# Optimization experiments

Hardware: AMD Instinct MI355X
Metric: run time of the kernel (lower is better)

## Reference

```python
import jax, jax.numpy as jnp
import numpy as np
from jax.ops import segment_sum

N_NODES = 100000


def gcn_conv(x, W, b, src, dst, num_nodes):
    # PyG GCNConv: h = x @ W; add self-loops; symmetric normalization; aggregate; + bias
    h = x @ W  # [N, out]
    # add self-loops
    loops = jnp.arange(num_nodes, dtype=src.dtype)
    src_sl = jnp.concatenate([src, loops])
    dst_sl = jnp.concatenate([dst, loops])
    # degree over destination (incl. self-loops), edge weight = 1
    deg = segment_sum(jnp.ones_like(src_sl, dtype=h.dtype), dst_sl, num_segments=num_nodes)
    dinv = jnp.where(deg > 0, jax.lax.rsqrt(deg), 0.0)
    norm = dinv[src_sl] * dinv[dst_sl]  # [E+N]
    msg = h[src_sl] * norm[:, None]      # gather + scale, [E+N, out]
    out = segment_sum(msg, dst_sl, num_segments=num_nodes)  # scatter-add
    return out + b


def setup_inputs() -> dict:
    key = jax.random.key(0)
    ks = jax.random.split(key, 5)
    N, F, C = N_NODES, 64, 10
    E = 1600000
    x = jax.random.normal(ks[0], (N, F), dtype=jnp.float32)
    edge_index = jax.random.randint(ks[1], (2, E), 0, N, dtype=jnp.int64)
    W1 = jax.random.normal(ks[2], (F, 128), dtype=jnp.float32) * (1.0 / np.sqrt(F))
    b1 = jnp.zeros((128,), dtype=jnp.float32)
    W2 = jax.random.normal(ks[3], (128, 16), dtype=jnp.float32) * (1.0 / np.sqrt(128))
    b2 = jnp.zeros((16,), dtype=jnp.float32)
    Wl = jax.random.normal(ks[4], (16, C), dtype=jnp.float32) * (1.0 / np.sqrt(16))
    bl = jnp.zeros((C,), dtype=jnp.float32)
    return {"x": x, "edge_index": edge_index, "W1": W1, "b1": b1,
            "W2": W2, "b2": b2, "Wl": Wl, "bl": bl}


def reference(x, edge_index, W1, b1, W2, b2, Wl, bl):
    src, dst = edge_index[0], edge_index[1]
    h = gcn_conv(x, W1, b1, src, dst, N_NODES)
    h = jax.nn.relu(h)
    h = gcn_conv(h, W2, b2, src, dst, N_NODES)
    h = jax.nn.relu(h)
    return h @ Wl + bl
```

## Files before the change

kernel.cpp:

```cpp
#include <hip/hip_runtime.h>
#include <hip/hip_fp16.h>


#define F_IN 64
#define H1DIM 128
#define H2DIM 16
#define C_OUT 10

#define NB 1024
#define BSZ_LOG 7
#define SC_PER_TH 16

typedef _Float16 f16x8 __attribute__((ext_vector_type(8)));
typedef _Float16 f16x4 __attribute__((ext_vector_type(4)));
typedef float f32x4 __attribute__((ext_vector_type(4)));

__global__ void bucket_count(const int* __restrict__ ei, int E,
                             int* __restrict__ bucket_cnt) {
    __shared__ int h[NB];
    for (int t = threadIdx.x; t < NB; t += blockDim.x) h[t] = 0;
    __syncthreads();
    int stride = gridDim.x * blockDim.x;
    for (int e = blockIdx.x * blockDim.x + threadIdx.x; e < E; e += stride) {
        int d = ei[E + e];
        atomicAdd(&h[d >> BSZ_LOG], 1);
    }
    __syncthreads();
    for (int t = threadIdx.x; t < NB; t += blockDim.x)
        if (h[t]) atomicAdd(&bucket_cnt[t], h[t]);
}

__global__ void bucket_scan(const int* __restrict__ bucket_cnt,
                            int* __restrict__ bucket_off,
                            int* __restrict__ bucket_cursor) {
    __shared__ int sh[NB];
    int tid = threadIdx.x;
    int v = bucket_cnt[tid];
    sh[tid] = v;
    __syncthreads();
#pragma unroll
    for (int off = 1; off < NB; off <<= 1) {
        int t = (tid >= off) ? sh[tid - off] : 0;
        __syncthreads();
        sh[tid] += t;
        __syncthreads();
    }
    int ex = sh[tid] - v;
    bucket_off[tid] = ex;
    bucket_cursor[tid] = ex;
    if (tid == NB - 1) bucket_off[NB] = sh[tid];
}

__global__ __launch_bounds__(256) void bucket_scatter(
        const int* __restrict__ ei, int E,
        int* __restrict__ bucket_cursor, unsigned long long* __restrict__ pairs) {
    __shared__ int cnt[NB];
    __shared__ int base[NB];
    for (int t = threadIdx.x; t < NB; t += 256) cnt[t] = 0;
    __syncthreads();

    long long chunk = (long long)blockIdx.x * (256 * SC_PER_TH);
    int s_[SC_PER_TH], d_[SC_PER_TH];
    int m = 0;
#pragma unroll
    for (int k = 0; k < SC_PER_TH; k++) {
        long long e = chunk + k * 256 + threadIdx.x;
        if (e < E) { s_[m] = ei[e]; d_[m] = ei[E + e]; m++; }
    }
    for (int k = 0; k < m; k++) atomicAdd(&cnt[d_[k] >> BSZ_LOG], 1);
    __syncthreads();
    for (int t = threadIdx.x; t < NB; t += 256) {
        int c = cnt[t];
        base[t] = c ? atomicAdd(&bucket_cursor[t], c) : 0;
        cnt[t] = 0;
    }
    __syncthreads();
    for (int k = 0; k < m; k++) {
        int b = d_[k] >> BSZ_LOG;
        int pos = base[b] + atomicAdd(&cnt[b], 1);
        pairs[pos] = ((unsigned long long)(unsigned)d_[k] << 32) | (unsigned)s_[k];
    }
}

__global__ __launch_bounds__(256) void build_csr_convert(
        const unsigned long long* __restrict__ pairs,
        const int* __restrict__ bucket_off,
        const float* __restrict__ x, int N,
        float* __restrict__ dinv, int* __restrict__ row_off,
        int* __restrict__ csr_src, __half2* __restrict__ xh2) {
    int b = blockIdx.x;
    int base_node = b << BSZ_LOG;
    int nn = min(128, N - base_node);
    __shared__ int cnt[128];
    __shared__ int sc[128];
    __shared__ int cur[128];
    __shared__ float sdi[128];
    int tid = threadIdx.x;
    if (tid < 128) cnt[tid] = 0;
    __syncthreads();

    int pbeg = bucket_off[b], pend = bucket_off[b + 1];
    for (int j = pbeg + tid; j < pend; j += 256)
        atomicAdd(&cnt[(int)(pairs[j] >> 32) - base_node], 1);
    __syncthreads();

    int v = (tid < 128) ? cnt[tid] : 0;
    if (tid < 128) sc[tid] = v;
    __syncthreads();
#pragma unroll
    for (int off = 1; off < 128; off <<= 1) {
        int t = (tid < 128 && tid >= off) ? sc[tid - off] : 0;
        __syncthreads();
        if (tid < 128) sc[tid] += t;
        __syncthreads();
    }
    if (tid < nn) {
        int ro = pbeg + sc[tid] - v;
        row_off[base_node + tid] = ro;
        cur[tid] = ro;
        float di = rsqrtf((float)(v + 1));
        dinv[base_node + tid] = di;
        sdi[tid] = di;
    }
    if (b == 0 && tid == 0) row_off[N] = bucket_off[NB];
    __syncthreads();

    for (int j = pbeg + tid; j < pend; j += 256) {
        unsigned long long p = pairs[j];
        int d = (int)(p >> 32), s = (int)(p & 0xffffffffu);
        int pos = atomicAdd(&cur[d - base_node], 1);
        csr_src[pos] = s;
    }

    const float2* x2 = (const float2*)x;
    int total = nn * 32;
    for (int t = tid; t < total; t += 256) {
        int nl = t >> 5, l = t & 31;
        float di = sdi[nl];
        long long idx = (long long)(base_node + nl) * 32 + l;
        float2 xv = x2[idx];
        xh2[idx] = __floats2half2_rn(xv.x * di, xv.y * di);
    }
}

__global__ __launch_bounds__(256) void gather1_h2(
        const f16x8* __restrict__ xh8, const float* __restrict__ dinv,
        const int* __restrict__ row_off, const int* __restrict__ csr_src,
        int N, f16x8* __restrict__ agg1h8) {
    int node = (blockIdx.x * 256 + threadIdx.x) >> 3;
    if (node >= N) return;
    int p = threadIdx.x & 7;
    int beg = row_off[node], end = row_off[node + 1];
    f16x8 self = xh8[(size_t)node * 8 + p];
    float acc[8];
#pragma unroll
    for (int q = 0; q < 8; q++) acc[q] = (float)self[q];
    int j = beg;
    for (; j + 4 <= end; j += 4) {
        int s0 = csr_src[j], s1 = csr_src[j + 1];
        int s2 = csr_src[j + 2], s3 = csr_src[j + 3];
        f16x8 v0 = xh8[(size_t)s0 * 8 + p];
        f16x8 v1 = xh8[(size_t)s1 * 8 + p];
        f16x8 v2 = xh8[(size_t)s2 * 8 + p];
        f16x8 v3 = xh8[(size_t)s3 * 8 + p];
#pragma unroll
        for (int q = 0; q < 8; q++)
            acc[q] += ((float)v0[q] + (float)v1[q]) + ((float)v2[q] + (float)v3[q]);
    }
    for (; j < end; ++j) {
        f16x8 v = xh8[(size_t)csr_src[j] * 8 + p];
#pragma unroll
        for (int q = 0; q < 8; q++) acc[q] += (float)v[q];
    }
    float di = dinv[node];
    f16x8 o;
#pragma unroll
    for (int q = 0; q < 8; q++) o[q] = (_Float16)(acc[q] * di);
    agg1h8[(size_t)node * 8 + p] = o;
}

__global__ __launch_bounds__(256) void pack_weights(
        const float* __restrict__ W1, const float* __restrict__ W2,
        f16x8* __restrict__ W1p, f16x8* __restrict__ W2p) {
    int s = blockIdx.x * 256 + threadIdx.x;
    if (s < 1024) {
        int frag = s >> 6, lane = s & 63;
        int tile = frag >> 1, kf = frag & 1;
        int c = lane & 15, g = lane >> 4;
        f16x8 v;
#pragma unroll
        for (int j = 0; j < 8; ++j)
            v[j] = (_Float16)W1[(kf * 32 + g * 8 + j) * H1DIM + tile * 16 + c];
        W1p[s] = v;
    } else if (s < 1024 + 256) {
        int s2 = s - 1024;
        int f = s2 >> 6, lane = s2 & 63;
        int c = lane & 15, g = lane >> 4;
        f16x8 v;
#pragma unroll
        for (int j = 0; j < 8; ++j)
            v[j] = (_Float16)W2[(f * 32 + g * 8 + j) * H2DIM + c];
        W2p[s2] = v;
    }
}

__global__ __launch_bounds__(256) void dense1_mfma(
        const _Float16* __restrict__ agg, const f16x8* __restrict__ W1p,
        const f16x8* __restrict__ W2p, const float* __restrict__ b1,
        const float* __restrict__ dinv, int N, _Float16* __restrict__ z2h) {
    __shared__ float sb1[H1DIM];
    __shared__ _Float16 Hl[4][16 * H1DIM];
    if (threadIdx.x < H1DIM) sb1[threadIdx.x] = b1[threadIdx.x];
    __syncthreads();
    const int wave = threadIdx.x >> 6, lane = threadIdx.x & 63;
    const int c = lane & 15, g = lane >> 4;
    const int nodeBase = blockIdx.x * 64 + wave * 16;

    int nld = nodeBase + c; if (nld > N - 1) nld = N - 1;
    const f16x8 a0 = *(const f16x8*)(agg + (size_t)nld * 64 + g * 8);
    const f16x8 a1 = *(const f16x8*)(agg + (size_t)nld * 64 + 32 + g * 8);

    _Float16* hl = Hl[wave];
    const f32x4 zero = {0.f, 0.f, 0.f, 0.f};
#pragma unroll
    for (int t = 0; t < 8; ++t) {
        f32x4 d = __builtin_amdgcn_mfma_f32_16x16x32_f16(W1p[(t * 2 + 1) * 64 + lane], a1, zero, 0, 0, 0);
        d = __builtin_amdgcn_mfma_f32_16x16x32_f16(W1p[(t * 2 + 0) * 64 + lane], a0, d, 0, 0, 0);
        f16x4 hv;
#pragma unroll
        for (int r = 0; r < 4; ++r)
            hv[r] = (_Float16)fmaxf(d[r] + sb1[t * 16 + g * 4 + r], 0.f);
        unsigned byte = ((unsigned)c * 256 + (unsigned)t * 32 + (unsigned)g * 8) ^ ((unsigned)(c & 7) << 4);
        *(f16x4*)((char*)hl + byte) = hv;
    }

    f32x4 acc = zero;
#pragma unroll
    for (int f = 0; f < 4; ++f) {
        unsigned byte = ((unsigned)c * 256 + (unsigned)f * 64 + (unsigned)g * 16) ^ ((unsigned)(c & 7) << 4);
        f16x8 a2 = *(const f16x8*)((char*)hl + byte);
        acc = __builtin_amdgcn_mfma_f32_16x16x32_f16(a2, W2p[f * 64 + lane], acc, 0, 0, 0);
    }
#pragma unroll
    for (int r = 0; r < 4; ++r) {
        int node = nodeBase + g * 4 + r;
        if (node < N) z2h[(size_t)node * 16 + c] = (_Float16)(acc[r] * dinv[node]);
    }
}

__global__ __launch_bounds__(256) void gather2_final_v2(
        const __half2* __restrict__ z2h, const float* __restrict__ dinv,
        const int* __restrict__ row_off, const int* __restrict__ csr_src,
        const float* __restrict__ b2, const float* __restrict__ Wl,
        const float* __restrict__ bl, int N, float* __restrict__ out) {
    __shared__ float sWl[H2DIM * C_OUT];
    __shared__ float sb2[H2DIM];
    __shared__ float sbl[C_OUT];
    __shared__ float hbuf[32][17];
    int tid = threadIdx.x;
    if (tid < H2DIM * C_OUT) sWl[tid] = Wl[tid];
    if (tid < H2DIM) sb2[tid] = b2[tid];
    if (tid < C_OUT) sbl[tid] = bl[tid];
    __syncthreads();

    int node = blockIdx.x * 32 + (tid >> 3);
    int p = tid & 7;
    int ln = tid >> 3;
    if (node < N) {
        int beg = row_off[node], end = row_off[node + 1];
        float2 sv = __half22float2(z2h[(size_t)node * 8 + p]);
        float ax = sv.x, ay = sv.y;
        int j = beg;
        for (; j + 4 <= end; j += 4) {
            int s0 = csr_src[j], s1 = csr_src[j + 1];
            int s2 = csr_src[j + 2], s3 = csr_src[j + 3];
            float2 v0 = __half22float2(z2h[(size_t)s0 * 8 + p]);
            float2 v1 = __half22float2(z2h[(size_t)s1 * 8 + p]);
            float2 v2 = __half22float2(z2h[(size_t)s2 * 8 + p]);
            float2 v3 = __half22float2(z2h[(size_t)s3 * 8 + p]);
            ax += (v0.x + v1.x) + (v2.x + v3.x);
            ay += (v0.y + v1.y) + (v2.y + v3.y);
        }
        for (; j < end; ++j) {
            float2 v = __half22float2(z2h[(size_t)csr_src[j] * 8 + p]);
            ax += v.x; ay += v.y;
        }
        float di = dinv[node];
        hbuf[ln][2 * p]     = fmaxf(ax * di + sb2[2 * p], 0.f);
        hbuf[ln][2 * p + 1] = fmaxf(ay * di + sb2[2 * p + 1], 0.f);
    }
    __syncthreads();
    if (node < N) {
        float o0 = sbl[p];
        float o1 = (p < 2) ? sbl[8 + p] : 0.f;
#pragma unroll
        for (int k = 0; k < H2DIM; k++) {
            float hk = hbuf[ln][k];
            o0 = fmaf(hk, sWl[k * C_OUT + p], o0);
            if (p < 2) o1 = fmaf(hk, sWl[k * C_OUT + 8 + p], o1);
        }
        out[(size_t)node * C_OUT + p] = o0;
        if (p < 2) out[(size_t)node * C_OUT + 8 + p] = o1;
    }
}

extern "C" void kernel_launch(void* const* d_in, const int* in_sizes, int n_in,
                              void* d_out, int out_size, void* d_ws, size_t ws_size,
                              hipStream_t stream) {
    const float* x  = (const float*)d_in[0];
    const int*   ei = (const int*)d_in[1];
    const float* W1 = (const float*)d_in[2];
    const float* b1 = (const float*)d_in[3];
    const float* W2 = (const float*)d_in[4];
    const float* b2 = (const float*)d_in[5];
    const float* Wl = (const float*)d_in[6];
    const float* bl = (const float*)d_in[7];
    float* out = (float*)d_out;

    const int N = in_sizes[0] / F_IN;
    const int E = in_sizes[1] / 2;

    size_t off = 0;
    auto carve = [&](size_t bytes) {
        void* p = (char*)d_ws + off;
        off += (bytes + 255) & ~(size_t)255;
        return p;
    };
    float*   dinv    = (float*)  carve((size_t)N * sizeof(float));
    int*     row_off = (int*)    carve(((size_t)N + 1) * sizeof(int));
    int*     csr_src = (int*)    carve((size_t)E * sizeof(int));
    __half2* xh2     = (__half2*)carve((size_t)N * 32 * sizeof(__half2));
    size_t agg_bytes = (size_t)N * 32 * sizeof(__half2);
    size_t pr_bytes  = (size_t)E * sizeof(unsigned long long);
    __half2* agg1h   = (__half2*)carve(agg_bytes > pr_bytes ? agg_bytes : pr_bytes);
    __half2* z2h     = (__half2*)carve((size_t)N * 8 * sizeof(__half2));
    int*     bcnt    = (int*)    carve(NB * sizeof(int));
    int*     boff    = (int*)    carve((NB + 1) * sizeof(int));
    int*     bcur    = (int*)    carve(NB * sizeof(int));
    f16x8*   W1p     = (f16x8*)  carve(1024 * sizeof(f16x8));
    f16x8*   W2p     = (f16x8*)  carve(256 * sizeof(f16x8));
    unsigned long long* pairs = (unsigned long long*)agg1h;

    const int nbuckets_used = (N + (1 << BSZ_LOG) - 1) >> BSZ_LOG;

    hipMemsetAsync(bcnt, 0, NB * sizeof(int), stream);
    pack_weights<<<5, 256, 0, stream>>>(W1, W2, W1p, W2p);
    bucket_count<<<208, 256, 0, stream>>>(ei, E, bcnt);
    bucket_scan<<<1, NB, 0, stream>>>(bcnt, boff, bcur);
    bucket_scatter<<<(E + 256 * SC_PER_TH - 1) / (256 * SC_PER_TH), 256, 0, stream>>>(
        ei, E, bcur, pairs);
    build_csr_convert<<<nbuckets_used, 256, 0, stream>>>(
        pairs, boff, x, N, dinv, row_off, csr_src, xh2);

    gather1_h2<<<((size_t)N * 8 + 255) / 256, 256, 0, stream>>>(
        (const f16x8*)xh2, dinv, row_off, csr_src, N, (f16x8*)agg1h);
    dense1_mfma<<<(N + 63) / 64, 256, 0, stream>>>(
        (const _Float16*)agg1h, W1p, W2p, b1, dinv, N, (_Float16*)z2h);
    gather2_final_v2<<<(N + 31) / 32, 256, 0, stream>>>(
        z2h, dinv, row_off, csr_src, b2, Wl, bl, N, out);
}
```

Baseline: 131.3 us.

## Pack CSR build pairs into 32-bit words and use larger 512-node buckets

After: 150.4 us. +14.6%, slower.

```diff
diff --git a/kernel.cpp b/kernel.cpp
--- a/kernel.cpp
+++ b/kernel.cpp
@@ -7,39 +7,42 @@
 #define H2DIM 16
 #define C_OUT 10
 
-#define NB 1024
-#define BSZ_LOG 7
+#define NBK 256
+#define BSZ_LOG 9
+#define BNODES 512
 #define SC_PER_TH 16
+#define SRC_BITS 17
 
 typedef _Float16 f16x8 __attribute__((ext_vector_type(8)));
 typedef _Float16 f16x4 __attribute__((ext_vector_type(4)));
 typedef float f32x4 __attribute__((ext_vector_type(4)));
 
-__global__ void bucket_count(const int* __restrict__ ei, int E,
+__global__ void bucket_count(const int* __restrict__ ei, int E, int N,
                              int* __restrict__ bucket_cnt) {
-    __shared__ int h[NB];
-    for (int t = threadIdx.x; t < NB; t += blockDim.x) h[t] = 0;
+    __shared__ int h[NBK];
+    for (int t = threadIdx.x; t < NBK; t += blockDim.x) h[t] = 0;
     __syncthreads();
     int stride = gridDim.x * blockDim.x;
     for (int e = blockIdx.x * blockDim.x + threadIdx.x; e < E; e += stride) {
-        int d = ei[E + e];
-        atomicAdd(&h[d >> BSZ_LOG], 1);
-    }
-    __syncthreads();
-    for (int t = threadIdx.x; t < NB; t += blockDim.x)
+        int s = ei[e], d = ei[E + e];
+        if ((unsigned)s < (unsigned)N && (unsigned)d < (unsigned)N)
+            atomicAdd(&h[d >> BSZ_LOG], 1);
+    }
+    __syncthreads();
+    for (int t = threadIdx.x; t < NBK; t += blockDim.x)
         if (h[t]) atomicAdd(&bucket_cnt[t], h[t]);
 }
 
 __global__ void bucket_scan(const int* __restrict__ bucket_cnt,
                             int* __restrict__ bucket_off,
                             int* __restrict__ bucket_cursor) {
-    __shared__ int sh[NB];
+    __shared__ int sh[NBK];
     int tid = threadIdx.x;
     int v = bucket_cnt[tid];
     sh[tid] = v;
     __syncthreads();
 #pragma unroll
-    for (int off = 1; off < NB; off <<= 1) {
+    for (int off = 1; off < NBK; off <<= 1) {
         int t = (tid >= off) ? sh[tid - off] : 0;
         __syncthreads();
         sh[tid] += t;
@@ -48,15 +51,15 @@
     int ex = sh[tid] - v;
     bucket_off[tid] = ex;
     bucket_cursor[tid] = ex;
-    if (tid == NB - 1) bucket_off[NB] = sh[tid];
+    if (tid == NBK - 1) bucket_off[NBK] = sh[tid];
 }
 
 __global__ __launch_bounds__(256) void bucket_scatter(
-        const int* __restrict__ ei, int E,
-        int* __restrict__ bucket_cursor, unsigned long long* __restrict__ pairs) {
-    __shared__ int cnt[NB];
-    __shared__ int base[NB];
-    for (int t = threadIdx.x; t < NB; t += 256) cnt[t] = 0;
+        const int* __restrict__ ei, int E, int N,
+        int* __restrict__ bucket_cursor, unsigned* __restrict__ pairs) {
+    __shared__ int cnt[NBK];
+    __shared__ int base[NBK];
+    for (int t = threadIdx.x; t < NBK; t += 256) cnt[t] = 0;
     __syncthreads();
 
     long long chunk = (long long)blockIdx.x * (256 * SC_PER_TH);
@@ -65,11 +68,16 @@
 #pragma unroll
     for (int k = 0; k < SC_PER_TH; k++) {
         long long e = chunk + k * 256 + threadIdx.x;
-        if (e < E) { s_[m] = ei[e]; d_[m] = ei[E + e]; m++; }
+        if (e < E) {
+            int s = ei[e], d = ei[E + e];
+            if ((unsigned)s < (unsigned)N && (unsigned)d < (unsigned)N) {
+                s_[m] = s; d_[m] = d; m++;
+            }
+        }
     }
     for (int k = 0; k < m; k++) atomicAdd(&cnt[d_[k] >> BSZ_LOG], 1);
     __syncthreads();
-    for (int t = threadIdx.x; t < NB; t += 256) {
+    for (int t = threadIdx.x; t < NBK; t += 256) {
         int c = cnt[t];
         base[t] = c ? atomicAdd(&bucket_cursor[t], c) : 0;
         cnt[t] = 0;
@@ -78,57 +86,64 @@
     for (int k = 0; k < m; k++) {
         int b = d_[k] >> BSZ_LOG;
         int pos = base[b] + atomicAdd(&cnt[b], 1);
-        pairs[pos] = ((unsigned long long)(unsigned)d_[k] << 32) | (unsigned)s_[k];
+        pairs[pos] = ((unsigned)(d_[k] & (BNODES - 1)) << SRC_BITS) | (unsigned)s_[k];
     }
 }
 
 __global__ __launch_bounds__(256) void build_csr_convert(
-        const unsigned long long* __restrict__ pairs,
+        const unsigned* __restrict__ pairs,
         const int* __restrict__ bucket_off,
         const float* __restrict__ x, int N,
         float* __restrict__ dinv, int* __restrict__ row_off,
         int* __restrict__ csr_src, __half2* __restrict__ xh2) {
     int b = blockIdx.x;
     int base_node = b << BSZ_LOG;
-    int nn = min(128, N - base_node);
-    __shared__ int cnt[128];
-    __shared__ int sc[128];
-    __shared__ int cur[128];
-    __shared__ float sdi[128];
+    int nn = min(BNODES, N - base_node);
+    __shared__ int cnt[BNODES];
+    __shared__ int cur[BNODES];
+    __shared__ float sdi[BNODES];
     int tid = threadIdx.x;
-    if (tid < 128) cnt[tid] = 0;
+    int i0 = tid, i1 = tid + 256;
+    cnt[i0] = 0; cnt[i1] = 0;
     __syncthreads();
 
     int pbeg = bucket_off[b], pend = bucket_off[b + 1];
     for (int j = pbeg + tid; j < pend; j += 256)
-        atomicAdd(&cnt[(int)(pairs[j] >> 32) - base_node], 1);
-    __syncthreads();
-
-    int v = (tid < 128) ? cnt[tid] : 0;
-    if (tid < 128) sc[tid] = v;
-    __syncthreads();
-#pragma unroll
-    for (int off = 1; off < 128; off <<= 1) {
-        int t = (tid < 128 && tid >= off) ? sc[tid - off] : 0;
+        atomicAdd(&cnt[pairs[j] >> SRC_BITS], 1);
+    __syncthreads();
+
+    int v0 = cnt[i0], v1 = cnt[i1];
+#pragma unroll
+    for (int off = 1; off < BNODES; off <<= 1) {
+        int a0 = (i0 >= off) ? cnt[i0 - off] : 0;
+        int a1 = (i1 >= off) ? cnt[i1 - off] : 0;
         __syncthreads();
-        if (tid < 128) sc[tid] += t;
+        cnt[i0] += a0; cnt[i1] += a1;
         __syncthreads();
     }
-    if (tid < nn) {
-        int ro = pbeg + sc[tid] - v;
-        row_off[base_node + tid] = ro;
-        cur[tid] = ro;
-        float di = rsqrtf((float)(v + 1));
-        dinv[base_node + tid] = di;
-        sdi[tid] = di;
-    }
-    if (b == 0 && tid == 0) row_off[N] = bucket_off[NB];
+    if (i0 < nn) {
+        int ro = pbeg + cnt[i0] - v0;
+        row_off[base_node + i0] = ro;
+        cur[i0] = ro;
+        float di = rsqrtf((float)(v0 + 1));
+        dinv[base_node + i0] = di;
+        sdi[i0] = di;
+    }
+    if (i1 < nn) {
+        int ro = pbeg + cnt[i1] - v1;
+        row_off[base_node + i1] = ro;
+        cur[i1] = ro;
+        float di = rsqrtf((float)(v1 + 1));
+        dinv[base_node + i1] = di;
+        sdi[i1] = di;
+    }
+    if (b == 0 && tid == 0) row_off[N] = bucket_off[NBK];
     __syncthreads();
 
     for (int j = pbeg + tid; j < pend; j += 256) {
-        unsigned long long p = pairs[j];
-        int d = (int)(p >> 32), s = (int)(p & 0xffffffffu);
-        int pos = atomicAdd(&cur[d - base_node], 1);
+        unsigned p = pairs[j];
+        int dl = p >> SRC_BITS, s = p & ((1u << SRC_BITS) - 1);
+        int pos = atomicAdd(&cur[dl], 1);
         csr_src[pos] = s;
     }
 
@@ -331,24 +346,24 @@
     int*     csr_src = (int*)    carve((size_t)E * sizeof(int));
     __half2* xh2     = (__half2*)carve((size_t)N * 32 * sizeof(__half2));
     size_t agg_bytes = (size_t)N * 32 * sizeof(__half2);
-    size_t pr_bytes  = (size_t)E * sizeof(unsigned long long);
+    size_t pr_bytes  = (size_t)E * sizeof(unsigned);
     __half2* agg1h   = (__half2*)carve(agg_bytes > pr_bytes ? agg_bytes : pr_bytes);
     __half2* z2h     = (__half2*)carve((size_t)N * 8 * sizeof(__half2));
-    int*     bcnt    = (int*)    carve(NB * sizeof(int));
-    int*     boff    = (int*)    carve((NB + 1) * sizeof(int));
-    int*     bcur    = (int*)    carve(NB * sizeof(int));
+    int*     bcnt    = (int*)    carve(NBK * sizeof(int));
+    int*     boff    = (int*)    carve((NBK + 1) * sizeof(int));
+    int*     bcur    = (int*)    carve(NBK * sizeof(int));
     f16x8*   W1p     = (f16x8*)  carve(1024 * sizeof(f16x8));
     f16x8*   W2p     = (f16x8*)  carve(256 * sizeof(f16x8));
-    unsigned long long* pairs = (unsigned long long*)agg1h;
-
-    const int nbuckets_used = (N + (1 << BSZ_LOG) - 1) >> BSZ_LOG;
-
-    hipMemsetAsync(bcnt, 0, NB * sizeof(int), stream);
+    unsigned* pairs = (unsigned*)agg1h;
+
+    const int nbuckets_used = (N + BNODES - 1) >> BSZ_LOG;
+
+    hipMemsetAsync(bcnt, 0, NBK * sizeof(int), stream);
     pack_weights<<<5, 256, 0, stream>>>(W1, W2, W1p, W2p);
-    bucket_count<<<208, 256, 0, stream>>>(ei, E, bcnt);
-    bucket_scan<<<1, NB, 0, stream>>>(bcnt, boff, bcur);
+    bucket_count<<<208, 256, 0, stream>>>(ei, E, N, bcnt);
+    bucket_scan<<<1, NBK, 0, stream>>>(bcnt, boff, bcur);
     bucket_scatter<<<(E + 256 * SC_PER_TH - 1) / (256 * SC_PER_TH), 256, 0, stream>>>(
-        ei, E, bcur, pairs);
+        ei, E, N, bcur, pairs);
     build_csr_convert<<<nbuckets_used, 256, 0, stream>>>(
         pairs, boff, x, N, dinv, row_off, csr_src, xh2);
 
```
